# Kernel optimization log

Hardware: AMD Instinct MI355X
Metric: run time of the kernel (lower is better)

## Reference

```python
import jax, jax.numpy as jnp
import numpy as np

N = 200000   # nodes
E = 3200000  # edges
G = 8192     # graphs
F_IN = 28    # one-hot node feature dim (dataset.num_node_features)
D = 50       # embed_dim
H = 16       # hidden_channels
C = 2        # num_classes


def setup_inputs() -> dict:
    key = jax.random.key(0)
    ks = jax.random.split(key, 12)
    x = jax.random.normal(ks[0], (N, F_IN), jnp.float32)
    row = jax.random.randint(ks[1], (E,), 0, N)   # source nodes (edge_index[0])
    col = jax.random.randint(ks[2], (E,), 0, N)   # target nodes (edge_index[1])
    edge_attr = jax.random.uniform(ks[3], (E,), jnp.float32)
    batch = jnp.sort(jax.random.randint(ks[4], (N,), 0, G))
    emb = jax.random.normal(ks[5], (F_IN, D), jnp.float32) * 0.1
    W1 = jax.random.normal(ks[6], (D, H), jnp.float32) * (1.0 / np.sqrt(D))
    b1 = jnp.zeros((H,), jnp.float32)
    W2 = jax.random.normal(ks[7], (H, H), jnp.float32) * (1.0 / np.sqrt(H))
    b2 = jnp.zeros((H,), jnp.float32)
    W3 = jax.random.normal(ks[8], (H, C), jnp.float32) * (1.0 / np.sqrt(H))
    b3 = jnp.zeros((C,), jnp.float32)
    return dict(x=x, row=row, col=col, edge_attr=edge_attr, batch=batch,
                emb=emb, W1=W1, b1=b1, W2=W2, b2=b2, W3=W3, b3=b3)


def gcn_conv(h, row, col, ew, W, b):
    """PyG GCNConv with normalize=True, add_self_loops=True (fill_value=1)."""
    # degree at target nodes, including self-loop weight 1
    deg = jax.ops.segment_sum(ew, col, num_segments=N) + 1.0
    dinv = jnp.where(deg > 0, deg ** -0.5, 0.0)
    hw = h @ W                                   # [N, out]
    norm = dinv[row] * ew * dinv[col]            # [E]
    agg = jax.ops.segment_sum(hw[row] * norm[:, None], col, num_segments=N)
    agg = agg + hw * (dinv * dinv)[:, None]      # self-loop contribution
    return agg + b


def reference(x, row, col, edge_attr, batch, emb, W1, b1, W2, b2, W3, b3):
    # x is one-hot-ish -> argmax -> embedding lookup
    h = emb[jnp.argmax(x, axis=1)]               # [N, D]
    h = jax.nn.relu(gcn_conv(h, row, col, edge_attr, W1, b1))
    # dropout is identity in eval mode
    h = jax.nn.relu(gcn_conv(h, row, col, edge_attr, W2, b2))
    h = gcn_conv(h, row, col, edge_attr, W3, b3)  # [N, C]
    # global mean pool over graphs
    sums = jax.ops.segment_sum(h, batch, num_segments=G)
    cnts = jax.ops.segment_sum(jnp.ones((N,), h.dtype), batch, num_segments=G)
    pooled = sums / jnp.maximum(cnts, 1.0)[:, None]  # [G, C]
    return jax.nn.softmax(pooled, axis=1)
```

## Files before the change

kernel.cpp:

```cpp
#include <hip/hip_runtime.h>
#include <hip/hip_fp16.h>

constexpr int Nn  = 200000;
constexpr int Ne  = 3200000;
constexpr int Ng  = 8192;
constexpr int FIN = 28;
constexpr int DE  = 50;
constexpr int HD  = 16;
constexpr int CD  = 2;

constexpr int NBIN   = (Nn + 255) >> 8;
constexpr int NBLK   = 512;
constexpr int CH     = Ne / NBLK;
constexpr int CSTR   = 800;
constexpr int LDSCAP = 4608;

__device__ __forceinline__ float dec_ea(unsigned u) {
  return ((float)(u & 16383u) + 0.5f) * (1.0f / 16384.0f);
}

__device__ __forceinline__ float2 dec8(unsigned short u) {
  __half lo = __ushort_as_half((unsigned short)((u & 0x00ffu) << 8));
  __half hi = __ushort_as_half((unsigned short)(u & 0xff00u));
  return make_float2(__half2float(lo), __half2float(hi));
}
__device__ __forceinline__ unsigned char enc8(float f) {
  unsigned short b = __half_as_ushort(__float2half(f));
  return (unsigned char)((unsigned short)(b + 0x0080u) >> 8);
}

static inline int nblocks(long long n, int bs = 256, int cap = 16384) {
  long long b = (n + bs - 1) / bs;
  return (int)(b < cap ? b : cap);
}

__global__ void k_zero(float* __restrict__ p, int n) {
  int i = blockIdx.x * blockDim.x + threadIdx.x;
  if (i < n) p[i] = 0.0f;
}

__global__ __launch_bounds__(256) void k_count(const int* __restrict__ col,
                                               int* __restrict__ counts) {
  __shared__ int c[NBIN];
  for (int i = threadIdx.x; i < NBIN; i += 256) c[i] = 0;
  __syncthreads();
  int lo = blockIdx.x * CH;
  for (int i = threadIdx.x; i < CH; i += 256) atomicAdd(&c[col[lo + i] >> 8], 1);
  __syncthreads();
  for (int i = threadIdx.x; i < NBIN; i += 256) counts[blockIdx.x * CSTR + i] = c[i];
}

__global__ __launch_bounds__(512) void k_scan1b(int* __restrict__ counts,
                                                int* __restrict__ colTotal) {
  __shared__ int s[NBLK];
  int bin = blockIdx.x, t = threadIdx.x;
  int v = counts[t * CSTR + bin];
  s[t] = v;
  __syncthreads();
  for (int d = 1; d < NBLK; d <<= 1) {
    int x = (t >= d) ? s[t - d] : 0;
    __syncthreads();
    s[t] += x;
    __syncthreads();
  }
  counts[t * CSTR + bin] = s[t] - v;
  if (t == NBLK - 1) colTotal[bin] = s[t];
}

__global__ __launch_bounds__(1024) void k_scanBins(const int* __restrict__ colTotal,
                                                   int* __restrict__ binBase,
                                                   int* __restrict__ start) {
  __shared__ int s[1024];
  int t = threadIdx.x;
  int v = (t < NBIN) ? colTotal[t] : 0;
  s[t] = v;
  __syncthreads();
  for (int d = 1; d < 1024; d <<= 1) {
    int x = (t >= d) ? s[t - d] : 0;
    __syncthreads();
    s[t] += x;
    __syncthreads();
  }
  if (t < NBIN) binBase[t] = s[t] - v;
  if (t == NBIN - 1) { binBase[NBIN] = s[t]; start[Nn] = s[t]; }
}

__global__ __launch_bounds__(256) void k_place(const int* __restrict__ row,
                                               const int* __restrict__ col,
                                               const float* __restrict__ ea,
                                               const int* __restrict__ counts,
                                               const int* __restrict__ binBase,
                                               unsigned long long* __restrict__ staged) {
  __shared__ unsigned long long stage[CH];
  __shared__ int lhist[NBIN];
  __shared__ int lcur[NBIN];
  __shared__ int gbase[NBIN];
  __shared__ int partial[256];
  int blk = blockIdx.x, t = threadIdx.x;
  int lo = blk * CH;
  for (int i = t; i < NBIN; i += 256) { lhist[i] = 0; lcur[i] = 0; }
  __syncthreads();
  for (int i = t; i < CH; i += 256) atomicAdd(&lhist[col[lo + i] >> 8], 1);
  __syncthreads();
  constexpr int CPT = (NBIN + 255) / 256;
  int b0 = t * CPT, s = 0;
#pragma unroll
  for (int j = 0; j < CPT; ++j) { int b = b0 + j; if (b < NBIN) s += lhist[b]; }
  partial[t] = s;
  __syncthreads();
  for (int d = 1; d < 256; d <<= 1) {
    int x = (t >= d) ? partial[t - d] : 0;
    __syncthreads();
    partial[t] += x;
    __syncthreads();
  }
  int run = partial[t] - s;
#pragma unroll
  for (int j = 0; j < CPT; ++j) {
    int b = b0 + j;
    if (b < NBIN) { int c = lhist[b]; lhist[b] = run; run += c; }
  }
  for (int i = t; i < NBIN; i += 256) gbase[i] = binBase[i] + counts[blk * CSTR + i];
  __syncthreads();
  for (int i = t; i < CH; i += 256) {
    int e = lo + i;
    int c = col[e], bin = c >> 8;
    unsigned q = (unsigned)__float2int_rd(ea[e] * 16384.0f);
    if (q > 16383u) q = 16383u;
    unsigned long long entry =
        ((unsigned long long)(unsigned)c << 32) | ((unsigned)row[e] << 14) | q;
    int pos = lhist[bin] + atomicAdd(&lcur[bin], 1);
    stage[pos] = entry;
  }
  __syncthreads();
  for (int i = t; i < CH; i += 256) {
    unsigned long long entry = stage[i];
    int bin = (int)(entry >> 40);
    staged[gbase[bin] + (i - lhist[bin])] = entry;
  }
}

__global__ void k_embw(const float* __restrict__ emb, const float* __restrict__ W1,
                       float* __restrict__ EW1) {
  int t = threadIdx.x;
  if (t < FIN * HD) {
    int i = t / HD, k = t % HD;
    float s = 0.0f;
    for (int j = 0; j < DE; ++j) s += emb[i * DE + j] * W1[j * HD + k];
    EW1[t] = s;
  }
}

__global__ __launch_bounds__(256) void k_finemb(const int* __restrict__ binBase,
                                                const unsigned long long* __restrict__ staged,
                                                const float* __restrict__ x,
                                                const float* __restrict__ EW1,
                                                unsigned* __restrict__ csr,
                                                int* __restrict__ start,
                                                float* __restrict__ dinv,
                                                unsigned char* __restrict__ hws1) {
  __shared__ int ncnt[256];
  __shared__ int noff[256];
  __shared__ int ncur[256];
  __shared__ float sdeg[256];
  __shared__ unsigned outb[LDSCAP];
  int b = blockIdx.x, t = threadIdx.x;
  int lo = binBase[b];
  int cnt = binBase[b + 1] - lo;
  if (cnt > LDSCAP) cnt = LDSCAP;
  ncnt[t] = 0; ncur[t] = 0; sdeg[t] = 0.0f;
  __syncthreads();
  for (int i = t; i < cnt; i += 256) {
    unsigned long long p = staged[lo + i];
    int cl = (int)((p >> 32) & 255u);
    atomicAdd(&ncnt[cl], 1);
    atomicAdd(&sdeg[cl], dec_ea((unsigned)p));
  }
  __syncthreads();
  int v = ncnt[t];
  noff[t] = v;
  __syncthreads();
  for (int d = 1; d < 256; d <<= 1) {
    int xsh = (t >= d) ? noff[t - d] : 0;
    __syncthreads();
    noff[t] += xsh;
    __syncthreads();
  }
  int excl = noff[t] - v;
  __syncthreads();
  noff[t] = excl;
  __syncthreads();
  for (int i = t; i < cnt; i += 256) {
    unsigned long long p = staged[lo + i];
    int cl = (int)((p >> 32) & 255u);
    int idx = noff[cl] + atomicAdd(&ncur[cl], 1);
    outb[idx] = (unsigned)p;
  }
  __syncthreads();
  for (int i = t; i < cnt; i += 256) csr[lo + i] = outb[i];
  int node = (b << 8) + t;
  if (node >= Nn) return;
  start[node] = lo + noff[t];
  float di = rsqrtf(sdeg[t] + 1.0f);
  dinv[node] = di;
  const float* xp = x + (long long)node * FIN;
  int arg = 0; float best = xp[0];
#pragma unroll
  for (int j = 1; j < FIN; ++j) { float vv = xp[j]; if (vv > best) { best = vv; arg = j; } }
  const float* ep = EW1 + arg * HD;
#pragma unroll
  for (int k = 0; k < HD; ++k) hws1[((size_t)node << 4) + k] = enc8(ep[k] * di);
}

template <int OUTC>
__global__ __launch_bounds__(256) void k_conv(const int* __restrict__ start,
                                              const unsigned* __restrict__ csr,
                                              const unsigned short* __restrict__ f8,
                                              const float* __restrict__ dinv,
                                              const float* __restrict__ bias,
                                              const float* __restrict__ Wn,
                                              void* __restrict__ outw) {
  int n = blockIdx.x * 4 + (threadIdx.x >> 6);
  if (n >= Nn) return;
  int lane = threadIdx.x & 63;
  int slot = lane >> 3;
  int p    = lane & 7;
  int lo = start[n], hi = start[n + 1];
  float ax = 0.0f, ay = 0.0f;
  for (int j = lo + slot; j < hi; j += 8) {
    unsigned u = __builtin_nontemporal_load(csr + j);
    int r = u >> 14;
    float w = dec_ea(u);
    float2 v = dec8(f8[(r << 3) + p]);
    ax = fmaf(v.x, w, ax);
    ay = fmaf(v.y, w, ay);
  }
#pragma unroll
  for (int d = 8; d < 64; d <<= 1) {
    ax += __shfl_xor(ax, d, 64);
    ay += __shfl_xor(ay, d, 64);
  }
  float di = dinv[n];
  float2 self = dec8(f8[(n << 3) + p]);
  float h0 = fmaxf(di * (ax + self.x) + bias[2 * p + 0], 0.0f);
  float h1 = fmaxf(di * (ay + self.y) + bias[2 * p + 1], 0.0f);
  int k = lane & 15;
  float acc2 = 0.0f;
#pragma unroll
  for (int q = 0; q < 8; ++q) {
    float hj0 = __shfl(h0, q, 64);
    float hj1 = __shfl(h1, q, 64);
    acc2 = fmaf(hj0, Wn[(2 * q + 0) * OUTC + (OUTC == 16 ? k : (k & 1))], acc2);
    acc2 = fmaf(hj1, Wn[(2 * q + 1) * OUTC + (OUTC == 16 ? k : (k & 1))], acc2);
  }
  acc2 *= di;
  if (OUTC == 16) {
    if (lane < 16) ((unsigned char*)outw)[((size_t)n << 4) + k] = enc8(acc2);
  } else {
    if (lane < CD) ((__half*)outw)[(size_t)n * CD + k] = __float2half(acc2);
  }
}

__global__ __launch_bounds__(256) void k_conv3pool(const int* __restrict__ start,
                                                   const unsigned* __restrict__ csr,
                                                   const __half* __restrict__ h3,
                                                   const float* __restrict__ dinv,
                                                   const float* __restrict__ b3,
                                                   const int* __restrict__ batch,
                                                   float* __restrict__ sums,
                                                   float* __restrict__ cnts) {
  int wid = threadIdx.x >> 6;
  int lane = threadIdx.x & 63;
  int nsub = lane >> 2;
  int slot = lane & 3;
  int n = (blockIdx.x * 4 + wid) * 16 + nsub;
  if (n >= Nn) return;
  const __half2* h2 = (const __half2*)h3;
  int lo = start[n], hi = start[n + 1];
  float ax = 0.0f, ay = 0.0f;
  for (int j = lo + slot; j < hi; j += 4) {
    unsigned u = __builtin_nontemporal_load(csr + j);
    int r = u >> 14;
    float w = dec_ea(u);
    float2 v = __half22float2(h2[r]);
    ax = fmaf(v.x, w, ax);
    ay = fmaf(v.y, w, ay);
  }
  ax += __shfl_xor(ax, 1, 64); ay += __shfl_xor(ay, 1, 64);
  ax += __shfl_xor(ax, 2, 64); ay += __shfl_xor(ay, 2, 64);
  if (slot == 0) {
    float di = dinv[n];
    float2 self = __half22float2(h2[n]);
    float a0 = di * (ax + self.x) + b3[0];
    float a1 = di * (ay + self.y) + b3[1];
    int g = batch[n];
    atomicAdd(&sums[2 * g + 0], a0);
    atomicAdd(&sums[2 * g + 1], a1);
    atomicAdd(&cnts[g], 1.0f);
  }
}

__global__ void k_softmax(const float* __restrict__ sums, const float* __restrict__ cnts,
                          float* __restrict__ out, int g) {
  int stride = gridDim.x * blockDim.x;
  for (int i = blockIdx.x * blockDim.x + threadIdx.x; i < g; i += stride) {
    float cnt = fmaxf(cnts[i], 1.0f);
    float c0 = sums[i * 2 + 0] / cnt;
    float c1 = sums[i * 2 + 1] / cnt;
    float m = fmaxf(c0, c1);
    float e0 = __expf(c0 - m), e1 = __expf(c1 - m);
    float inv = 1.0f / (e0 + e1);
    out[i * 2 + 0] = e0 * inv;
    out[i * 2 + 1] = e1 * inv;
  }
}

extern "C" void kernel_launch(void* const* d_in, const int* in_sizes, int n_in,
                              void* d_out, int out_size, void* d_ws, size_t ws_size,
                              hipStream_t stream) {
  const float* x   = (const float*)d_in[0];
  const int*   row = (const int*)d_in[1];
  const int*   col = (const int*)d_in[2];
  const float* ea  = (const float*)d_in[3];
  const int*   bat = (const int*)d_in[4];
  const float* emb = (const float*)d_in[5];
  const float* W1  = (const float*)d_in[6];
  const float* b1  = (const float*)d_in[7];
  const float* W2  = (const float*)d_in[8];
  const float* b2  = (const float*)d_in[9];
  const float* W3  = (const float*)d_in[10];
  const float* b3  = (const float*)d_in[11];
  float* out = (float*)d_out;

  float* ws = (float*)d_ws;
  size_t o = 0;
  float* sums    = ws + o; o += (size_t)Ng * CD;
  float* cnts    = ws + o; o += Ng;
  float* dinv    = ws + o; o += Nn;
  float* EW1     = ws + o; o += FIN * HD + 16;
  int*   counts  = (int*)(ws + o); o += (size_t)NBLK * CSTR;
  int*   colTot  = (int*)(ws + o); o += CSTR;
  int*   binBase = (int*)(ws + o); o += 1024;
  int*   startp  = (int*)(ws + o); o += Nn + 16;
  unsigned long long* staged = (unsigned long long*)(ws + o); o += (size_t)Ne * 2;
  unsigned* csr  = (unsigned*)(ws + o); o += (size_t)Ne;
  unsigned char* hws1 = (unsigned char*)(ws + o); o += (size_t)Nn * HD / 4;
  unsigned char* hws2 = (unsigned char*)(ws + o); o += (size_t)Nn * HD / 4;
  __half* hw3s   = (__half*)(ws + o); o += (size_t)Nn * CD / 2;
  (void)ws_size; (void)n_in; (void)in_sizes; (void)out_size;

  const int BS = 256;

  k_zero<<<nblocks(Ng * (CD + 1)), BS, 0, stream>>>(sums, Ng * (CD + 1));
  k_embw<<<1, 512, 0, stream>>>(emb, W1, EW1);

  k_count<<<NBLK, 256, 0, stream>>>(col, counts);
  k_scan1b<<<NBIN, NBLK, 0, stream>>>(counts, colTot);
  k_scanBins<<<1, 1024, 0, stream>>>(colTot, binBase, startp);
  k_place<<<NBLK, 256, 0, stream>>>(row, col, ea, counts, binBase, staged);
  k_finemb<<<NBIN, 256, 0, stream>>>(binBase, staged, x, EW1, csr, startp, dinv, hws1);

  k_conv<16><<<(Nn + 3) / 4, 256, 0, stream>>>(startp, csr, (const unsigned short*)hws1,
                                               dinv, b1, W2, hws2);
  k_conv<2><<<(Nn + 3) / 4, 256, 0, stream>>>(startp, csr, (const unsigned short*)hws2,
                                              dinv, b2, W3, hw3s);

  k_conv3pool<<<(Nn + 63) / 64, 256, 0, stream>>>(startp, csr, hw3s, dinv, b3, bat, sums, cnts);

  k_softmax<<<nblocks(Ng), BS, 0, stream>>>(sums, cnts, out, Ng);
}
```

Measured before the change: 443.1 us.

## Fold small kernels, reuse scanned counts, and unroll gather loops with grid-stride

The separate zero and embedding-weight kernels are folded into existing launches (an extra block of k_count computes EW1, and k_scanBins clears the pooling accumulators). k_place rebuilds its local histogram from the already-scanned counts instead of re-reading col with atomics. The conv and pool kernels become grid-stride loops that issue the first three edge loads per slot together to get more memory-level parallelism. k_conv3pool now uses 8 lanes per node instead of 4. These changes cut launches and redundant passes over col, at the cost of more registers and clamped dummy loads.

```diff
diff --git a/kernel.cpp b/kernel.cpp
--- a/kernel.cpp
+++ b/kernel.cpp
@@ -34,13 +34,21 @@
   return (int)(b < cap ? b : cap);
 }
 
-__global__ void k_zero(float* __restrict__ p, int n) {
-  int i = blockIdx.x * blockDim.x + threadIdx.x;
-  if (i < n) p[i] = 0.0f;
-}
-
 __global__ __launch_bounds__(256) void k_count(const int* __restrict__ col,
-                                               int* __restrict__ counts) {
+                                               int* __restrict__ counts,
+                                               const float* __restrict__ emb,
+                                               const float* __restrict__ W1,
+                                               float* __restrict__ EW1) {
+  if (blockIdx.x == NBLK) {
+    int t = threadIdx.x;
+    for (int u = t; u < FIN * HD; u += 256) {
+      int i = u / HD, k = u % HD;
+      float s = 0.0f;
+      for (int j = 0; j < DE; ++j) s += emb[i * DE + j] * W1[j * HD + k];
+      EW1[u] = s;
+    }
+    return;
+  }
   __shared__ int c[NBIN];
   for (int i = threadIdx.x; i < NBIN; i += 256) c[i] = 0;
   __syncthreads();
@@ -69,7 +77,10 @@
 
 __global__ __launch_bounds__(1024) void k_scanBins(const int* __restrict__ colTotal,
                                                    int* __restrict__ binBase,
-                                                   int* __restrict__ start) {
+                                                   int* __restrict__ start,
+                                                   float* __restrict__ zeroreg,
+                                                   int nzero) {
+  for (int i = threadIdx.x; i < nzero; i += 1024) zeroreg[i] = 0.0f;
   __shared__ int s[1024];
   int t = threadIdx.x;
   int v = (t < NBIN) ? colTotal[t] : 0;
@@ -89,6 +100,7 @@
                                                const int* __restrict__ col,
                                                const float* __restrict__ ea,
                                                const int* __restrict__ counts,
+                                               const int* __restrict__ colTotal,
                                                const int* __restrict__ binBase,
                                                unsigned long long* __restrict__ staged) {
   __shared__ unsigned long long stage[CH];
@@ -98,9 +110,13 @@
   __shared__ int partial[256];
   int blk = blockIdx.x, t = threadIdx.x;
   int lo = blk * CH;
-  for (int i = t; i < NBIN; i += 256) { lhist[i] = 0; lcur[i] = 0; }
-  __syncthreads();
-  for (int i = t; i < CH; i += 256) atomicAdd(&lhist[col[lo + i] >> 8], 1);
+  for (int i = t; i < NBIN; i += 256) {
+    int cur = counts[blk * CSTR + i];
+    int nxt = (blk == NBLK - 1) ? colTotal[i] : counts[(blk + 1) * CSTR + i];
+    lhist[i] = nxt - cur;
+    lcur[i] = 0;
+    gbase[i] = binBase[i] + cur;
+  }
   __syncthreads();
   constexpr int CPT = (NBIN + 255) / 256;
   int b0 = t * CPT, s = 0;
@@ -120,7 +136,6 @@
     int b = b0 + j;
     if (b < NBIN) { int c = lhist[b]; lhist[b] = run; run += c; }
   }
-  for (int i = t; i < NBIN; i += 256) gbase[i] = binBase[i] + counts[blk * CSTR + i];
   __syncthreads();
   for (int i = t; i < CH; i += 256) {
     int e = lo + i;
@@ -137,17 +152,6 @@
     unsigned long long entry = stage[i];
     int bin = (int)(entry >> 40);
     staged[gbase[bin] + (i - lhist[bin])] = entry;
-  }
-}
-
-__global__ void k_embw(const float* __restrict__ emb, const float* __restrict__ W1,
-                       float* __restrict__ EW1) {
-  int t = threadIdx.x;
-  if (t < FIN * HD) {
-    int i = t / HD, k = t % HD;
-    float s = 0.0f;
-    for (int j = 0; j < DE; ++j) s += emb[i * DE + j] * W1[j * HD + k];
-    EW1[t] = s;
   }
 }
 
@@ -220,44 +224,56 @@
                                               const float* __restrict__ bias,
                                               const float* __restrict__ Wn,
                                               void* __restrict__ outw) {
-  int n = blockIdx.x * 4 + (threadIdx.x >> 6);
-  if (n >= Nn) return;
   int lane = threadIdx.x & 63;
   int slot = lane >> 3;
   int p    = lane & 7;
-  int lo = start[n], hi = start[n + 1];
-  float ax = 0.0f, ay = 0.0f;
-  for (int j = lo + slot; j < hi; j += 8) {
-    unsigned u = __builtin_nontemporal_load(csr + j);
-    int r = u >> 14;
-    float w = dec_ea(u);
-    float2 v = dec8(f8[(r << 3) + p]);
-    ax = fmaf(v.x, w, ax);
-    ay = fmaf(v.y, w, ay);
-  }
-#pragma unroll
-  for (int d = 8; d < 64; d <<= 1) {
-    ax += __shfl_xor(ax, d, 64);
-    ay += __shfl_xor(ay, d, 64);
-  }
-  float di = dinv[n];
-  float2 self = dec8(f8[(n << 3) + p]);
-  float h0 = fmaxf(di * (ax + self.x) + bias[2 * p + 0], 0.0f);
-  float h1 = fmaxf(di * (ay + self.y) + bias[2 * p + 1], 0.0f);
-  int k = lane & 15;
-  float acc2 = 0.0f;
-#pragma unroll
-  for (int q = 0; q < 8; ++q) {
-    float hj0 = __shfl(h0, q, 64);
-    float hj1 = __shfl(h1, q, 64);
-    acc2 = fmaf(hj0, Wn[(2 * q + 0) * OUTC + (OUTC == 16 ? k : (k & 1))], acc2);
-    acc2 = fmaf(hj1, Wn[(2 * q + 1) * OUTC + (OUTC == 16 ? k : (k & 1))], acc2);
-  }
-  acc2 *= di;
-  if (OUTC == 16) {
-    if (lane < 16) ((unsigned char*)outw)[((size_t)n << 4) + k] = enc8(acc2);
-  } else {
-    if (lane < CD) ((__half*)outw)[(size_t)n * CD + k] = __float2half(acc2);
+  int k    = lane & 15;
+  int nstep = gridDim.x * 4;
+  for (int n = blockIdx.x * 4 + (threadIdx.x >> 6); n < Nn; n += nstep) {
+    int lo = start[n], hi = start[n + 1];
+    int j0 = lo + slot;
+    bool e0 = j0 < hi, e1 = j0 + 8 < hi, e2 = j0 + 16 < hi;
+    unsigned u0 = __builtin_nontemporal_load(csr + (e0 ? j0 : 0));
+    unsigned u1 = __builtin_nontemporal_load(csr + (e1 ? j0 + 8 : 0));
+    unsigned u2 = __builtin_nontemporal_load(csr + (e2 ? j0 + 16 : 0));
+    float w0 = e0 ? dec_ea(u0) : 0.0f;
+    float w1 = e1 ? dec_ea(u1) : 0.0f;
+    float w2 = e2 ? dec_ea(u2) : 0.0f;
+    float2 v0 = dec8(f8[((u0 >> 14) << 3) + p]);
+    float2 v1 = dec8(f8[((u1 >> 14) << 3) + p]);
+    float2 v2 = dec8(f8[((u2 >> 14) << 3) + p]);
+    float ax = fmaf(v2.x, w2, fmaf(v1.x, w1, v0.x * w0));
+    float ay = fmaf(v2.y, w2, fmaf(v1.y, w1, v0.y * w0));
+    for (int j = j0 + 24; j < hi; j += 8) {
+      unsigned u = __builtin_nontemporal_load(csr + j);
+      float w = dec_ea(u);
+      float2 v = dec8(f8[((u >> 14) << 3) + p]);
+      ax = fmaf(v.x, w, ax);
+      ay = fmaf(v.y, w, ay);
+    }
+#pragma unroll
+    for (int d = 8; d < 64; d <<= 1) {
+      ax += __shfl_xor(ax, d, 64);
+      ay += __shfl_xor(ay, d, 64);
+    }
+    float di = dinv[n];
+    float2 self = dec8(f8[((size_t)n << 3) + p]);
+    float h0 = fmaxf(di * (ax + self.x) + bias[2 * p + 0], 0.0f);
+    float h1 = fmaxf(di * (ay + self.y) + bias[2 * p + 1], 0.0f);
+    float acc2 = 0.0f;
+#pragma unroll
+    for (int q = 0; q < 8; ++q) {
+      float hj0 = __shfl(h0, q, 64);
+      float hj1 = __shfl(h1, q, 64);
+      acc2 = fmaf(hj0, Wn[(2 * q + 0) * OUTC + (OUTC == 16 ? k : (k & 1))], acc2);
+      acc2 = fmaf(hj1, Wn[(2 * q + 1) * OUTC + (OUTC == 16 ? k : (k & 1))], acc2);
+    }
+    acc2 *= di;
+    if (OUTC == 16) {
+      if (lane < 16) ((unsigned char*)outw)[((size_t)n << 4) + k] = enc8(acc2);
+    } else {
+      if (lane < CD) ((__half*)outw)[(size_t)n * CD + k] = __float2half(acc2);
+    }
   }
 }
 
@@ -269,34 +285,49 @@
                                                    const int* __restrict__ batch,
                                                    float* __restrict__ sums,
                                                    float* __restrict__ cnts) {
-  int wid = threadIdx.x >> 6;
+  const __half2* h2 = (const __half2*)h3;
   int lane = threadIdx.x & 63;
-  int nsub = lane >> 2;
-  int slot = lane & 3;
-  int n = (blockIdx.x * 4 + wid) * 16 + nsub;
-  if (n >= Nn) return;
-  const __half2* h2 = (const __half2*)h3;
-  int lo = start[n], hi = start[n + 1];
-  float ax = 0.0f, ay = 0.0f;
-  for (int j = lo + slot; j < hi; j += 4) {
-    unsigned u = __builtin_nontemporal_load(csr + j);
-    int r = u >> 14;
-    float w = dec_ea(u);
-    float2 v = __half22float2(h2[r]);
-    ax = fmaf(v.x, w, ax);
-    ay = fmaf(v.y, w, ay);
-  }
-  ax += __shfl_xor(ax, 1, 64); ay += __shfl_xor(ay, 1, 64);
-  ax += __shfl_xor(ax, 2, 64); ay += __shfl_xor(ay, 2, 64);
-  if (slot == 0) {
-    float di = dinv[n];
-    float2 self = __half22float2(h2[n]);
-    float a0 = di * (ax + self.x) + b3[0];
-    float a1 = di * (ay + self.y) + b3[1];
-    int g = batch[n];
-    atomicAdd(&sums[2 * g + 0], a0);
-    atomicAdd(&sums[2 * g + 1], a1);
-    atomicAdd(&cnts[g], 1.0f);
+  int nsub = lane >> 3;
+  int slot = lane & 7;
+  int wid  = threadIdx.x >> 6;
+  int nstep = gridDim.x * 32;
+  for (int nb = (blockIdx.x * 4 + wid) * 8; nb < Nn; nb += nstep) {
+    int n = nb + nsub;
+    int nn = min(n, Nn - 1);
+    int lo = start[nn], hi = start[nn + 1];
+    int j0 = lo + slot;
+    bool e0 = j0 < hi, e1 = j0 + 8 < hi, e2 = j0 + 16 < hi;
+    unsigned u0 = __builtin_nontemporal_load(csr + (e0 ? j0 : 0));
+    unsigned u1 = __builtin_nontemporal_load(csr + (e1 ? j0 + 8 : 0));
+    unsigned u2 = __builtin_nontemporal_load(csr + (e2 ? j0 + 16 : 0));
+    float w0 = e0 ? dec_ea(u0) : 0.0f;
+    float w1 = e1 ? dec_ea(u1) : 0.0f;
+    float w2 = e2 ? dec_ea(u2) : 0.0f;
+    float2 v0 = __half22float2(h2[u0 >> 14]);
+    float2 v1 = __half22float2(h2[u1 >> 14]);
+    float2 v2 = __half22float2(h2[u2 >> 14]);
+    float ax = fmaf(v2.x, w2, fmaf(v1.x, w1, v0.x * w0));
+    float ay = fmaf(v2.y, w2, fmaf(v1.y, w1, v0.y * w0));
+    for (int j = j0 + 24; j < hi; j += 8) {
+      unsigned u = __builtin_nontemporal_load(csr + j);
+      float w = dec_ea(u);
+      float2 v = __half22float2(h2[u >> 14]);
+      ax = fmaf(v.x, w, ax);
+      ay = fmaf(v.y, w, ay);
+    }
+    ax += __shfl_xor(ax, 1, 64); ay += __shfl_xor(ay, 1, 64);
+    ax += __shfl_xor(ax, 2, 64); ay += __shfl_xor(ay, 2, 64);
+    ax += __shfl_xor(ax, 4, 64); ay += __shfl_xor(ay, 4, 64);
+    if (slot == 0 && n < Nn) {
+      float di = dinv[n];
+      float2 self = __half22float2(h2[n]);
+      float a0 = di * (ax + self.x) + b3[0];
+      float a1 = di * (ay + self.y) + b3[1];
+      int g = batch[n];
+      atomicAdd(&sums[2 * g + 0], a0);
+      atomicAdd(&sums[2 * g + 1], a1);
+      atomicAdd(&cnts[g], 1.0f);
+    }
   }
 }
 
@@ -349,23 +380,19 @@
   __half* hw3s   = (__half*)(ws + o); o += (size_t)Nn * CD / 2;
   (void)ws_size; (void)n_in; (void)in_sizes; (void)out_size;
 
-  const int BS = 256;
-
-  k_zero<<<nblocks(Ng * (CD + 1)), BS, 0, stream>>>(sums, Ng * (CD + 1));
-  k_embw<<<1, 512, 0, stream>>>(emb, W1, EW1);
-
-  k_count<<<NBLK, 256, 0, stream>>>(col, counts);
+  k_count<<<NBLK + 1, 256, 0, stream>>>(col, counts, emb, W1, EW1);
   k_scan1b<<<NBIN, NBLK, 0, stream>>>(counts, colTot);
-  k_scanBins<<<1, 1024, 0, stream>>>(colTot, binBase, startp);
-  k_place<<<NBLK, 256, 0, stream>>>(row, col, ea, counts, binBase, staged);
+  k_scanBins<<<1, 1024, 0, stream>>>(colTot, binBase, startp, sums, Ng * (CD + 1));
+  k_place<<<NBLK, 256, 0, stream>>>(row, col, ea, counts, colTot, binBase, staged);
   k_finemb<<<NBIN, 256, 0, stream>>>(binBase, staged, x, EW1, csr, startp, dinv, hws1);
 
-  k_conv<16><<<(Nn + 3) / 4, 256, 0, stream>>>(startp, csr, (const unsigned short*)hws1,
-                                               dinv, b1, W2, hws2);
-  k_conv<2><<<(Nn + 3) / 4, 256, 0, stream>>>(startp, csr, (const unsigned short*)hws2,
-                                              dinv, b2, W3, hw3s);
-
-  k_conv3pool<<<(Nn + 63) / 64, 256, 0, stream>>>(startp, csr, hw3s, dinv, b3, bat, sums, cnts);
-
-  k_softmax<<<nblocks(Ng), BS, 0, stream>>>(sums, cnts, out, Ng);
-}
+  k_conv<16><<<nblocks((long long)Nn * 64), 256, 0, stream>>>(
+      startp, csr, (const unsigned short*)hws1, dinv, b1, W2, hws2);
+  k_conv<2><<<nblocks((long long)Nn * 64), 256, 0, stream>>>(
+      startp, csr, (const unsigned short*)hws2, dinv, b2, W3, hw3s);
+
+  k_conv3pool<<<nblocks((long long)Nn * 8), 256, 0, stream>>>(
+      startp, csr, hw3s, dinv, b3, bat, sums, cnts);
+
+  k_softmax<<<nblocks(Ng), 256, 0, stream>>>(sums, cnts, out, Ng);
+}
```

Result: faster. 394.8 us (-10.9%).
